# Optimization experiments

Measured on AMD Instinct MI355X. Metric: run time of the kernel, lower is better.

Reference implementation:

```python
import jax, jax.numpy as jnp
import numpy as np

N = 16384        # num nodes
NE = 262144      # num edges (avg degree 16)
IN = 3           # input_dim
H = 128          # hidden_dim
ED = 2           # edge_dim (position differences, 2D coords)
L = 3            # num GNN layers
LAT = 64         # latent_dim
NR = 8192        # num reduced nodes (reduction_factor=0.5)
K = 3            # kNN for interpolation


def _ln(x, g, b, eps=1e-5):
    m = jnp.mean(x, axis=-1, keepdims=True)
    v = jnp.mean((x - m) ** 2, axis=-1, keepdims=True)
    return (x - m) / jnp.sqrt(v + eps) * g + b


def _mlp(x, w1, b1, w2, b2):
    return jax.nn.relu(x @ w1 + b1) @ w2 + b2


def setup_inputs() -> dict:
    key = jax.random.key(0)
    ks = jax.random.split(key, 32)
    def nrm(k, shape, s=0.05):
        return jax.random.normal(k, shape, dtype=jnp.float32) * s
    inp = {}
    inp["x"] = jax.random.normal(ks[0], (N, IN), dtype=jnp.float32)
    inp["node_positions"] = jax.random.uniform(ks[1], (N, 2), dtype=jnp.float32)
    inp["edge_index"] = jax.random.randint(ks[2], (2, NE), 0, N, dtype=jnp.int32)
    # mlp0 + lnm0
    inp["m0_w1"] = nrm(ks[3], (IN, H)); inp["m0_b1"] = jnp.zeros((H,), jnp.float32)
    inp["m0_w2"] = nrm(ks[4], (H, H)); inp["m0_b2"] = jnp.zeros((H,), jnp.float32)
    inp["ln0_g"] = jnp.ones((H,), jnp.float32); inp["ln0_b"] = jnp.zeros((H,), jnp.float32)
    # mlp1 + lnm1 (edge feature transform, edge_dim=2)
    inp["m1_w1"] = nrm(ks[5], (ED, H)); inp["m1_b1"] = jnp.zeros((H,), jnp.float32)
    inp["m1_w2"] = nrm(ks[6], (H, ED)); inp["m1_b2"] = jnp.zeros((ED,), jnp.float32)
    inp["ln1_g"] = jnp.ones((ED,), jnp.float32); inp["ln1_b"] = jnp.zeros((ED,), jnp.float32)
    # GNN layers (stacked over L)
    inp["g_msg_w1"] = nrm(ks[7], (L, 2 * H + ED, H)); inp["g_msg_b1"] = jnp.zeros((L, H), jnp.float32)
    inp["g_msg_w2"] = nrm(ks[8], (L, H, H)); inp["g_msg_b2"] = jnp.zeros((L, H), jnp.float32)
    inp["g_node_w1"] = nrm(ks[9], (L, 2 * H, H)); inp["g_node_b1"] = jnp.zeros((L, H), jnp.float32)
    inp["g_node_w2"] = nrm(ks[10], (L, H, H)); inp["g_node_b2"] = jnp.zeros((L, H), jnp.float32)
    inp["g_edge_w1"] = nrm(ks[11], (L, 2 * H + ED, H)); inp["g_edge_b1"] = jnp.zeros((L, H), jnp.float32)
    inp["g_edge_w2"] = nrm(ks[12], (L, H, ED)); inp["g_edge_b2"] = jnp.zeros((L, ED), jnp.float32)
    inp["g_lnn_g"] = jnp.ones((L, H), jnp.float32); inp["g_lnn_b"] = jnp.zeros((L, H), jnp.float32)
    inp["g_lne_g"] = jnp.ones((L, ED), jnp.float32); inp["g_lne_b"] = jnp.zeros((L, ED), jnp.float32)
    # mlp2 + lnm2
    inp["m2_w1"] = nrm(ks[13], (H, H)); inp["m2_b1"] = jnp.zeros((H,), jnp.float32)
    inp["m2_w2"] = nrm(ks[14], (H, H)); inp["m2_b2"] = jnp.zeros((H,), jnp.float32)
    inp["ln2_g"] = jnp.ones((H,), jnp.float32); inp["ln2_b"] = jnp.zeros((H,), jnp.float32)
    # output_proj
    inp["op_w1"] = nrm(ks[15], (H, H)); inp["op_b1"] = jnp.zeros((H,), jnp.float32)
    inp["op_w2"] = nrm(ks[16], (H, LAT)); inp["op_b2"] = jnp.zeros((LAT,), jnp.float32)
    return inp


def reference(x, edge_index, node_positions,
              m0_w1, m0_b1, m0_w2, m0_b2, ln0_g, ln0_b,
              m1_w1, m1_b1, m1_w2, m1_b2, ln1_g, ln1_b,
              g_msg_w1, g_msg_b1, g_msg_w2, g_msg_b2,
              g_node_w1, g_node_b1, g_node_w2, g_node_b2,
              g_edge_w1, g_edge_b1, g_edge_w2, g_edge_b2,
              g_lnn_g, g_lnn_b, g_lne_g, g_lne_b,
              m2_w1, m2_b1, m2_w2, m2_b2, ln2_g, ln2_b,
              op_w1, op_b1, op_w2, op_b2):
    row, col = edge_index[0], edge_index[1]
    # Stage 1: node encoder  U0 -> U1
    u = _ln(_mlp(x, m0_w1, m0_b1, m0_w2, m0_b2), ln0_g, ln0_b)
    # Stage 2: edge features from positions, E0 -> E1
    e = node_positions[col] - node_positions[row]          # [NE, 2]
    e = _ln(_mlp(e, m1_w1, m1_b1, m1_w2, m1_b2), ln1_g, ln1_b)
    # Stage 3: message-passing layers
    ones = jnp.ones((NE, 1), dtype=u.dtype)
    cnt = jnp.maximum(jax.ops.segment_sum(ones, col, num_segments=N), 1.0)
    for l in range(L):
        msg_in = jnp.concatenate([u[row], u[col], e], axis=-1)   # [NE, 2H+ED]
        m = _mlp(msg_in, g_msg_w1[l], g_msg_b1[l], g_msg_w2[l], g_msg_b2[l])
        agg = jax.ops.segment_sum(m, col, num_segments=N) / cnt  # mean aggregation
        u = _ln(u + _mlp(jnp.concatenate([u, agg], axis=-1),
                         g_node_w1[l], g_node_b1[l], g_node_w2[l], g_node_b2[l]),
                g_lnn_g[l], g_lnn_b[l])
        e = _ln(e + _mlp(jnp.concatenate([u[row], u[col], e], axis=-1),
                         g_edge_w1[l], g_edge_b1[l], g_edge_w2[l], g_edge_b2[l]),
                g_lne_g[l], g_lne_b[l])
    # Stage 4: U2 -> U3
    u3 = _ln(_mlp(u, m2_w1, m2_b1, m2_w2, m2_b2), ln2_g, ln2_b)
    # Stage 5: interpolate onto reduced coordinates (kNN inverse-distance weights)
    idx_r = jnp.floor(jnp.linspace(0.0, N - 1, NR)).astype(jnp.int32)
    x2 = node_positions[idx_r]                               # [NR, 2]
    d2 = (jnp.sum(x2 * x2, axis=1)[:, None]
          + jnp.sum(node_positions * node_positions, axis=1)[None, :]
          - 2.0 * x2 @ node_positions.T)                     # [NR, N]
    d2 = jnp.maximum(d2, 0.0)
    neg_d2, knn = jax.lax.top_k(-d2, K)                      # [NR, K]
    w = 1.0 / (jnp.sqrt(-neg_d2) + 1e-8)
    w = w / jnp.sum(w, axis=1, keepdims=True)
    z_feat = jnp.einsum('nk,nkh->nh', w, u3[knn])            # [NR, H]
    # Stage 6: global mean pool (no batch vector) + output projection
    z = jnp.mean(z_feat, axis=0, keepdims=True)              # [1, H]
    return _mlp(z, op_w1, op_b1, op_w2, op_b2)               # [1, LAT]
```

## Files before the change

kernel.cpp:

```cpp
#include <hip/hip_runtime.h>
#include <cfloat>

#define NN     16384
#define NEDGE  262144
#define HD     128
#define NLAYER 3
#define NRED   8192
#define LATD   64
#define GDIM   32

typedef __attribute__((ext_vector_type(8))) short short8;
typedef __attribute__((ext_vector_type(4))) float f32x4;

__device__ __forceinline__ unsigned short f2bf(float f) {
    union { float f; unsigned u; } v; v.f = f;
    unsigned u = v.u;
    unsigned r = u + 0x7fff + ((u >> 16) & 1);
    return (unsigned short)(r >> 16);
}
__device__ __forceinline__ void unp8(uint4 v, float* f) {
    unsigned w0=v.x, w1=v.y, w2=v.z, w3=v.w;
    f[0]=__uint_as_float(w0<<16); f[1]=__uint_as_float(w0&0xffff0000u);
    f[2]=__uint_as_float(w1<<16); f[3]=__uint_as_float(w1&0xffff0000u);
    f[4]=__uint_as_float(w2<<16); f[5]=__uint_as_float(w2&0xffff0000u);
    f[6]=__uint_as_float(w3<<16); f[7]=__uint_as_float(w3&0xffff0000u);
}
__device__ __forceinline__ unsigned long long umin64(unsigned long long a, unsigned long long b) {
    return a < b ? a : b;
}
__device__ __forceinline__ unsigned long long umax64(unsigned long long a, unsigned long long b) {
    return a < b ? b : a;
}

__device__ __forceinline__ unsigned short pack_std(const float* W, int ksteps, int q) {
    int j    = q & 7;
    int lane = (q >> 3) & 63;
    int ks   = (q >> 9) % ksteps;
    int nt   = q / (ksteps * 512);
    int k = ks*32 + (lane >> 4)*8 + j;
    int n = nt*16 + (lane & 15);
    return f2bf(W[k*128 + n]);
}
__device__ __forceinline__ unsigned short pack_w2e(const float* W, int q) {
    int j    = q & 7;
    int lane = (q >> 3) & 63;
    int ks   = q >> 9;
    int k = ks*32 + (lane >> 4)*8 + j;
    int n = lane & 15;
    return (n < 2) ? f2bf(W[k*2 + n]) : (unsigned short)0;
}

#define PK_TOTAL 448512
__global__ __launch_bounds__(256) void k_pack_all(
    const float* __restrict__ msgw1, const float* __restrict__ msgw2,
    const float* __restrict__ edgew1, const float* __restrict__ nodew1,
    const float* __restrict__ nodew2, const float* __restrict__ edgew2,
    const float* __restrict__ m0w2, const float* __restrict__ m2w1,
    const float* __restrict__ m2w2, unsigned short* __restrict__ P)
{
    int p = blockIdx.x*256 + threadIdx.x;
    if (p >= PK_TOTAL) return;
    unsigned short v;
    if (p < 98304) {
        int l = p / 32768, q = p % 32768;
        v = pack_std(msgw1 + (size_t)l*258*128, 8, q);
    } else if (p < 147456) {
        int t = p - 98304; int l = t / 16384, q = t % 16384;
        v = pack_std(msgw2 + (size_t)l*16384, 4, q);
    } else if (p < 245760) {
        int t = p - 147456; int l = t / 32768, q = t % 32768;
        v = pack_std(edgew1 + (size_t)l*258*128, 8, q);
    } else if (p < 344064) {
        int t = p - 245760; int l = t / 32768, q = t % 32768;
        v = pack_std(nodew1 + (size_t)l*256*128, 8, q);
    } else if (p < 393216) {
        int t = p - 344064; int l = t / 16384, q = t % 16384;
        v = pack_std(nodew2 + (size_t)l*16384, 4, q);
    } else if (p < 399360) {
        int t = p - 393216; int l = t / 2048, q = t % 2048;
        v = pack_w2e(edgew2 + (size_t)l*256, q);
    } else if (p < 415744) {
        v = pack_std(m0w2, 4, p - 399360);
    } else if (p < 432128) {
        v = pack_std(m2w1, 4, p - 415744);
    } else {
        v = pack_std(m2w2, 4, p - 432128);
    }
    P[p] = v;
}

union HUu { unsigned short Hs[64][136]; uint4 UF4[1024]; };

__global__ __launch_bounds__(256) void k_nenc_mfma(
    const float* __restrict__ x,
    const float* __restrict__ w1, const float* __restrict__ b1,
    const unsigned short* __restrict__ W2p, const float* __restrict__ B2,
    const float* __restrict__ lg, const float* __restrict__ lb,
    const unsigned short* __restrict__ mW1p, const float* __restrict__ mB1,
    float* __restrict__ u, unsigned short* __restrict__ u16,
    unsigned short* __restrict__ RM, unsigned short* __restrict__ CM,
    float* __restrict__ agg)
{
    __shared__ float xs[64][4];
    __shared__ float w1s[3][128];
    __shared__ float b1s[128];
    __shared__ HUu HU;
    __shared__ float Rs[64][132];
    __shared__ float red[64][4];
    __shared__ float mstat[64], sstat[64];
    int tid = threadIdx.x;
    int n0  = blockIdx.x * 64;
    {
        float4 z; z.x=0.f; z.y=0.f; z.z=0.f; z.w=0.f;
        for (int t = tid; t < 2048; t += 256)
            *(float4*)(agg + (size_t)(n0 + (t>>5))*HD + (t&31)*4) = z;
    }
    for (int t = tid; t < 384; t += 256) w1s[t >> 7][t & 127] = w1[t];
    if (tid < 128) b1s[tid] = b1[tid];
    for (int t = tid; t < 192; t += 256) xs[t/3][t%3] = x[(size_t)n0*3 + t];
    __syncthreads();
    {
        int m = tid >> 2, p0 = (tid & 3) * 32;
        float x0 = xs[m][0], x1 = xs[m][1], x2 = xs[m][2];
        for (int j = p0; j < p0 + 32; j += 2) {
            float h0 = fmaxf(b1s[j]   + x0*w1s[0][j]   + x1*w1s[1][j]   + x2*w1s[2][j],   0.f);
            float h1 = fmaxf(b1s[j+1] + x0*w1s[0][j+1] + x1*w1s[1][j+1] + x2*w1s[2][j+1], 0.f);
            *(unsigned*)&HU.Hs[m][j] = f2bf(h0) | ((unsigned)f2bf(h1) << 16);
        }
    }
    __syncthreads();

    int lane = tid & 63, wave = tid >> 6;
    int lr = lane & 15, lq = lane >> 4;
    f32x4 acc[8];
    #pragma unroll
    for (int i = 0; i < 8; ++i) acc[i] = (f32x4){0.f,0.f,0.f,0.f};
    for (int ks = 0; ks < 4; ++ks) {
        short8 a0 = *(const short8*)&HU.Hs[ 0 + lr][ks*32 + lq*8];
        short8 a1 = *(const short8*)&HU.Hs[16 + lr][ks*32 + lq*8];
        short8 a2 = *(const short8*)&HU.Hs[32 + lr][ks*32 + lq*8];
        short8 a3 = *(const short8*)&HU.Hs[48 + lr][ks*32 + lq*8];
        short8 b0 = *(const short8*)(W2p + (size_t)(((wave*2+0)*4 + ks)*64 + lane)*8);
        short8 b1v= *(const short8*)(W2p + (size_t)(((wave*2+1)*4 + ks)*64 + lane)*8);
        acc[0] = __builtin_amdgcn_mfma_f32_16x16x32_bf16(a0, b0, acc[0], 0,0,0);
        acc[1] = __builtin_amdgcn_mfma_f32_16x16x32_bf16(a0, b1v, acc[1], 0,0,0);
        acc[2] = __builtin_amdgcn_mfma_f32_16x16x32_bf16(a1, b0, acc[2], 0,0,0);
        acc[3] = __builtin_amdgcn_mfma_f32_16x16x32_bf16(a1, b1v, acc[3], 0,0,0);
        acc[4] = __builtin_amdgcn_mfma_f32_16x16x32_bf16(a2, b0, acc[4], 0,0,0);
        acc[5] = __builtin_amdgcn_mfma_f32_16x16x32_bf16(a2, b1v, acc[5], 0,0,0);
        acc[6] = __builtin_amdgcn_mfma_f32_16x16x32_bf16(a3, b0, acc[6], 0,0,0);
        acc[7] = __builtin_amdgcn_mfma_f32_16x16x32_bf16(a3, b1v, acc[7], 0,0,0);
    }
    #pragma unroll
// ... 5 lines not shown
            f32x4 v = acc[mt*2 + b];
            #pragma unroll
            for (int r = 0; r < 4; ++r) {
                int m = mt*16 + lq*4 + r;
                Rs[m][n] = v[r] + bb;
            }
        }
    }
    __syncthreads();
    {
        int m = tid >> 2, p = tid & 3;
        float s = 0.f;
        #pragma unroll 8
        for (int i = 0; i < 32; ++i) s += Rs[m][p*32 + i];
        red[m][p] = s;
    }
    __syncthreads();
    if (tid < 64) mstat[tid] = (red[tid][0]+red[tid][1]+red[tid][2]+red[tid][3]) * (1.f/HD);
    __syncthreads();
    {
        int m = tid >> 2, p = tid & 3;
        float mm = mstat[m];
        float s = 0.f;
        #pragma unroll 8
        for (int i = 0; i < 32; ++i) { float d = Rs[m][p*32 + i] - mm; s += d*d; }
        red[m][p] = s;
    }
    __syncthreads();
    if (tid < 64) sstat[tid] = sqrtf((red[tid][0]+red[tid][1]+red[tid][2]+red[tid][3]) * (1.f/HD) + 1e-5f);
    __syncthreads();
    for (int t = tid; t < 2048; t += 256) {
        int m = t >> 5, q = t & 31;
        int n = q*4;
        float mm = mstat[m], sd = sstat[m];
        float4 g4 = *(const float4*)(lg + n);
        float4 b4 = *(const float4*)(lb + n);
        float o0 = (Rs[m][n+0]-mm)/sd*g4.x + b4.x;
        float o1 = (Rs[m][n+1]-mm)/sd*g4.y + b4.y;
        float o2 = (Rs[m][n+2]-mm)/sd*g4.z + b4.z;
        float o3 = (Rs[m][n+3]-mm)/sd*g4.w + b4.w;
        float4 fo; fo.x=o0; fo.y=o1; fo.z=o2; fo.w=o3;
        *(float4*)(u + (size_t)(n0+m)*HD + n) = fo;
        uint2 pk; pk.x = f2bf(o0) | (f2bf(o1)<<16); pk.y = f2bf(o2) | (f2bf(o3)<<16);
        *(uint2*)(u16 + (size_t)(n0+m)*HD + n) = pk;
        int ksf = n >> 5, sub = (n >> 3) & 3;
        int slot = (ksf*4 + (m >> 4))*64 + ((m & 15) | (sub << 4));
        unsigned short* UF = (unsigned short*)HU.UF4;
        *(uint2*)&UF[slot*8 + (n & 7)] = pk;
    }
    __syncthreads();

    for (int g = 0; g < 2; ++g) {
        int ksOff = g*4;
        unsigned short* Out = g ? CM : RM;
        #pragma unroll
        for (int i = 0; i < 8; ++i) acc[i] = (f32x4){0.f,0.f,0.f,0.f};
        for (int ks = 0; ks < 4; ++ks) {
            short8 a0 = *(const short8*)&HU.UF4[(ks*4+0)*64 + lane];
            short8 a1 = *(const short8*)&HU.UF4[(ks*4+1)*64 + lane];
            short8 a2 = *(const short8*)&HU.UF4[(ks*4+2)*64 + lane];
            short8 a3 = *(const short8*)&HU.UF4[(ks*4+3)*64 + lane];
            short8 b0 = *(const short8*)(mW1p + (size_t)(((wave*2+0)*8 + ksOff + ks)*64 + lane)*8);
            short8 b1v= *(const short8*)(mW1p + (size_t)(((wave*2+1)*8 + ksOff + ks)*64 + lane)*8);
            acc[0] = __builtin_amdgcn_mfma_f32_16x16x32_bf16(a0, b0, acc[0], 0,0,0);
            acc[1] = __builtin_amdgcn_mfma_f32_16x16x32_bf16(a0, b1v, acc[1], 0,0,0);
            acc[2] = __builtin_amdgcn_mfma_f32_16x16x32_bf16(a1, b0, acc[2], 0,0,0);
            acc[3] = __builtin_amdgcn_mfma_f32_16x16x32_bf16(a1, b1v, acc[3], 0,0,0);
            acc[4] = __builtin_amdgcn_mfma_f32_16x16x32_bf16(a2, b0, acc[4], 0,0,0);
            acc[5] = __builtin_amdgcn_mfma_f32_16x16x32_bf16(a2, b1v, acc[5], 0,0,0);
            acc[6] = __builtin_amdgcn_mfma_f32_16x16x32_bf16(a3, b0, acc[6], 0,0,0);
            acc[7] = __builtin_amdgcn_mfma_f32_16x16x32_bf16(a3, b1v, acc[7], 0,0,0);
        }
        #pragma unroll
        for (int b = 0; b < 2; ++b) {
            int n = (wave*2 + b)*16 + lr;
            float bb = g ? mB1[n] : 0.f;
            #pragma unroll
            for (int mt = 0; mt < 4; ++mt) {
                f32x4 v = acc[mt*2 + b];
                #pragma unroll
                for (int r = 0; r < 4; ++r) {
                    int rowp = n0 + mt*16 + lq*4 + r;
                    unsigned hv = f2bf(v[r] + bb);
                    unsigned ph = (unsigned)__shfl_xor((int)hv, 1, 64);
                    if (!(lr & 1))
                        *(unsigned*)&Out[(size_t)rowp*HD + n] = hv | (ph << 16);
                }
            }
        }
    }
}

__global__ __launch_bounds__(256) void k_edge_enc(
    const float* __restrict__ pos, const int* __restrict__ row, const int* __restrict__ col,
    const float* __restrict__ w1, const float* __restrict__ b1,
    const float* __restrict__ w2, const float* __restrict__ b2,
    const float* __restrict__ lg, const float* __restrict__ lb,
    float* __restrict__ ef)
{
    int e = blockIdx.x*256 + threadIdx.x;
    if (e >= NEDGE) return;
    int r = row[e], c = col[e];
    float e0 = pos[c*2]   - pos[r*2];
    float e1 = pos[c*2+1] - pos[r*2+1];
    float o0 = b2[0], o1 = b2[1];
    for (int j = 0; j < HD; ++j) {
        float h = fmaxf(e0*w1[j] + e1*w1[HD+j] + b1[j], 0.f);
        o0 += h*w2[j*2];
        o1 += h*w2[j*2+1];
    }
    float m  = 0.5f*(o0 + o1);
    float d0 = o0 - m, d1 = o1 - m;
    float v  = 0.5f*(d0*d0 + d1*d1);
    float sd = sqrtf(v + 1e-5f);
    ef[e*2]   = d0/sd*lg[0] + lb[0];
    ef[e*2+1] = d1/sd*lg[1] + lb[1];
}

__global__ void k_count2(const int* __restrict__ col, const float* __restrict__ pos,
                         int* __restrict__ cnt, int* __restrict__ gcnt)
{
    int e = blockIdx.x*256 + threadIdx.x;
    if (e < NEDGE) atomicAdd(&cnt[col[e]], 1);
    if (e < NN) {
        int cx = min(max((int)(pos[e*2]  *(float)GDIM), 0), GDIM-1);
        int cy = min(max((int)(pos[e*2+1]*(float)GDIM), 0), GDIM-1);
        atomicAdd(&gcnt[cy*GDIM + cx], 1);
    }
}

__global__ __launch_bounds__(256) void k_scan2(
    const int* __restrict__ cnt, int* __restrict__ head,
    const int* __restrict__ gcnt, int* __restrict__ gstart, int* __restrict__ ghead)
{
    __shared__ int ls[257];
    int tid = threadIdx.x;
    if (blockIdx.x == 0) {
        int base = tid * (NN/256);
        int s = 0;
// ... 52 lines not shown
    const float2* __restrict__ psort, const int* __restrict__ pidx,
    float* __restrict__ coef)
{
    int r = blockIdx.x*256 + threadIdx.x;
    int ni = (int)(2.0*r + (double)r/8191.0);
    float qx = pos[ni*2], qy = pos[ni*2+1];
    float s2 = qx*qx + qy*qy;
    int cx = min(max((int)(qx*(float)GDIM), 0), GDIM-1);
    int cy = min(max((int)(qy*(float)GDIM), 0), GDIM-1);
    const float h = 1.f/(float)GDIM;
    unsigned long long k0 = ~0ull, k1 = ~0ull, k2 = ~0ull;
    for (int rr = 0; rr < GDIM; ++rr) {
        if (rr > 0 && k2 != ~0ull) {
            float bound = rr*h;
            float d3 = __uint_as_float((unsigned)(k2 >> 32));
            if (d3 < bound*bound*0.9999f) break;
        }
        int ylo = max(cy-rr, 0), yhi = min(cy+rr, GDIM-1);
        int xlo = max(cx-rr, 0), xhi = min(cx+rr, GDIM-1);
        for (int gy = ylo; gy <= yhi; ++gy) {
            bool yedge = (gy == cy-rr) || (gy == cy+rr);
            for (int gx = xlo; gx <= xhi; ++gx) {
                if (!yedge && gx != cx-rr && gx != cx+rr) continue;
                int cell = gy*GDIM + gx;
                int s = gstart[cell], e = gstart[cell+1];
                for (; s < e; ++s) {
                    float2 p = psort[s];
                    float sc = p.x*p.x + p.y*p.y;
                    float dt = qx*p.x + qy*p.y;
                    float d2 = fmaxf(s2 + sc - 2.f*dt, 0.f);
                    unsigned long long key =
                        ((unsigned long long)__float_as_uint(d2) << 32) | (unsigned)pidx[s];
                    unsigned long long a0 = umin64(k0, key);
                    unsigned long long a1 = umin64(k1, umax64(k0, key));
                    unsigned long long a2 = umin64(k2, umax64(k1, key));
                    k0 = a0; k1 = a1; k2 = a2;
                }
            }
        }
    }
    float d0 = __uint_as_float((unsigned)(k0 >> 32));
    float d1 = __uint_as_float((unsigned)(k1 >> 32));
    float d2 = __uint_as_float((unsigned)(k2 >> 32));
    float w0 = 1.f/(sqrtf(d0) + 1e-8f);
    float w1 = 1.f/(sqrtf(d1) + 1e-8f);
    float w2 = 1.f/(sqrtf(d2) + 1e-8f);
    float ws = w0 + w1 + w2;
    atomicAdd(&coef[(int)(unsigned)(k0 & 0xffffffffu)], w0/ws);
    atomicAdd(&coef[(int)(unsigned)(k1 & 0xffffffffu)], w1/ws);
    atomicAdd(&coef[(int)(unsigned)(k2 & 0xffffffffu)], w2/ws);
}

__global__ __launch_bounds__(256) void k_hagg0(
    const unsigned short* __restrict__ RM, const unsigned short* __restrict__ CM,
    const float* __restrict__ ef,
    const int* __restrict__ row, const int* __restrict__ col,
    const int* __restrict__ perm,
    const float* __restrict__ mW1e,
    float* __restrict__ agg)
{
    __shared__ float Ms[64][132];
    __shared__ float Pw[256];
    __shared__ float Es[64][2];
    __shared__ int colS[64], rowS[64], eS[64];
    int tid = threadIdx.x;
    int e0  = blockIdx.x * 64;
    if (tid < 64) {
        int e = perm[e0 + tid];
        eS[tid] = e; colS[tid] = col[e]; rowS[tid] = row[e];
    }
    for (int t = tid; t < 256; t += 256) Pw[t] = mW1e[t];
    __syncthreads();
    if (tid < 128) { Es[tid>>1][tid&1] = ef[(size_t)eS[tid>>1]*2 + (tid&1)]; }
    __syncthreads();

    int mP = (tid >> 6)*16 + (tid & 15);
    int ccB = ((tid & 63) >> 4)*8;
    float e0v = Es[mP][0], e1v = Es[mP][1];
    #pragma unroll
    for (int s4 = 0; s4 < 4; ++s4) {
        int cc = s4*32 + ccB;
        uint4 ra = *(const uint4*)(RM + (size_t)rowS[mP]*HD + cc);
        uint4 cb = *(const uint4*)(CM + (size_t)colS[mP]*HD + cc);
        float rf[8], cf[8];
        unp8(ra, rf); unp8(cb, cf);
        float4 o0, o1;
        o0.x = fmaxf(rf[0]+cf[0]+e0v*Pw[cc+0]+e1v*Pw[128+cc+0], 0.f);
        o0.y = fmaxf(rf[1]+cf[1]+e0v*Pw[cc+1]+e1v*Pw[128+cc+1], 0.f);
        o0.z = fmaxf(rf[2]+cf[2]+e0v*Pw[cc+2]+e1v*Pw[128+cc+2], 0.f);
        o0.w = fmaxf(rf[3]+cf[3]+e0v*Pw[cc+3]+e1v*Pw[128+cc+3], 0.f);
        o1.x = fmaxf(rf[4]+cf[4]+e0v*Pw[cc+4]+e1v*Pw[128+cc+4], 0.f);
        o1.y = fmaxf(rf[5]+cf[5]+e0v*Pw[cc+5]+e1v*Pw[128+cc+5], 0.f);
        o1.z = fmaxf(rf[6]+cf[6]+e0v*Pw[cc+6]+e1v*Pw[128+cc+6], 0.f);
        o1.w = fmaxf(rf[7]+cf[7]+e0v*Pw[cc+7]+e1v*Pw[128+cc+7], 0.f);
        *(float4*)&Ms[mP][cc]   = o0;
        *(float4*)&Ms[mP][cc+4] = o1;
    }
    __syncthreads();

    {
        int n = tid & 127, hh = tid >> 7;
        int m0 = hh*32;
        float accv = 0.f;
        int cur = colS[m0];
        for (int m = m0; m < m0 + 32; ++m) {
            int cm = colS[m];
            if (cm != cur) {
                atomicAdd(&agg[(size_t)cur*HD + n], accv);
                accv = 0.f; cur = cm;
            }
            accv += Ms[m][n];
        }
        atomicAdd(&agg[(size_t)cur*HD + n], accv);
    }
}

union MsHFu { uint4 HF4[1024]; float Ms[64][132]; };

__global__ __launch_bounds__(256) void k_edgemsg2(
    const unsigned short* __restrict__ RE, const unsigned short* __restrict__ CE,
    const unsigned short* __restrict__ RM, const unsigned short* __restrict__ CM,
    float* __restrict__ ef,
    const int* __restrict__ row, const int* __restrict__ col,
    const int* __restrict__ perm,
    const float* __restrict__ eW1e,
    const unsigned short* __restrict__ eW2p, const float* __restrict__ eB2,
    const float* __restrict__ elg, const float* __restrict__ elb,
    const float* __restrict__ mW1e,
    float* __restrict__ agg, int writeEf)
{
    __shared__ MsHFu MU;
    __shared__ float Pew[256], Pmw[256];
    __shared__ float Es[64][2];
    __shared__ int colS[64], rowS[64], eS[64];
    int tid = threadIdx.x;
    int e0  = blockIdx.x * 64;
    if (tid < 64) {
        int e = perm[e0 + tid];
        eS[tid] = e; colS[tid] = col[e]; rowS[tid] = row[e];
    }
    for (int t = tid; t < 256; t += 256) { Pew[t] = eW1e[t]; Pmw[t] = mW1e[t]; }
    __syncthreads();

    int mP = (tid >> 6)*16 + (tid & 15);
    int ccB = ((tid & 63) >> 4)*8;
    uint4 regR[4], regC[4];
    #pragma unroll
    for (int s4 = 0; s4 < 4; ++s4) {
        int cc = s4*32 + ccB;
        regR[s4] = *(const uint4*)(RM + (size_t)rowS[mP]*HD + cc);
        regC[s4] = *(const uint4*)(CM + (size_t)colS[mP]*HD + cc);
    }
    if (tid < 128) { Es[tid>>1][tid&1] = ef[(size_t)eS[tid>>1]*2 + (tid&1)]; }
    __syncthreads();

    int lane = tid & 63, wave = tid >> 6;
    int lr = lane & 15, lq = lane >> 4;

    {
        float e0v = Es[mP][0], e1v = Es[mP][1];
        #pragma unroll
        for (int s4 = 0; s4 < 4; ++s4) {
            int s = tid + s4*256;
            int cc = s4*32 + ccB;
            uint4 ra = *(const uint4*)(RE + (size_t)rowS[mP]*HD + cc);
            uint4 cb = *(const uint4*)(CE + (size_t)colS[mP]*HD + cc);
            float rf[8], cf[8];
            unp8(ra, rf); unp8(cb, cf);
            unsigned short hb[8];
            #pragma unroll
            for (int j = 0; j < 8; ++j) {
                int n = cc + j;
                float o = rf[j] + cf[j] + e0v*Pew[n] + e1v*Pew[128+n];
                hb[j] = f2bf(fmaxf(o, 0.f));
            }
            uint4 pk;
            pk.x = hb[0] | ((unsigned)hb[1]<<16); pk.y = hb[2] | ((unsigned)hb[3]<<16);
            pk.z = hb[4] | ((unsigned)hb[5]<<16); pk.w = hb[6] | ((unsigned)hb[7]<<16);
            MU.HF4[s] = pk;
        }
    }
    __syncthreads();

    f32x4 a2 = (f32x4){0.f,0.f,0.f,0.f};
    for (int ks = 0; ks < 4; ++ks) {
        short8 a = *(const short8*)&MU.HF4[(ks*4 + wave)*64 + lane];
        short8 b = *(const short8*)(eW2p + (size_t)(ks*64 + lane)*8);
        a2 = __builtin_amdgcn_mfma_f32_16x16x32_bf16(a, b, a2, 0,0,0);
    }
    if (lr < 2) {
        int d = lr;
        float bb = eB2[d];
        float gg = elg[d], bl = elb[d];
        #pragma unroll
        for (int r = 0; r < 4; ++r) {
            int m = wave*16 + lq*4 + r;
            float rv = Es[m][d] + a2[r] + bb;
            float other = __shfl_xor(rv, 1, 64);
            float mm = 0.5f*(rv + other);
            float dr = rv - mm, dro = other - mm;
            float vv = 0.5f*(dr*dr + dro*dro);
            float outv = dr / sqrtf(vv + 1e-5f) * gg + bl;
            Es[m][d] = outv;
            if (writeEf) ef[(size_t)eS[m]*2 + d] = outv;
        }
    }
    __syncthreads();

    {
        float e0v = Es[mP][0], e1v = Es[mP][1];
        #pragma unroll
        for (int s4 = 0; s4 < 4; ++s4) {
            int cc = s4*32 + ccB;
            float rf[8], cf[8];
            unp8(regR[s4], rf); unp8(regC[s4], cf);
            float4 o0, o1;
            o0.x = fmaxf(rf[0]+cf[0]+e0v*Pmw[cc+0]+e1v*Pmw[128+cc+0], 0.f);
            o0.y = fmaxf(rf[1]+cf[1]+e0v*Pmw[cc+1]+e1v*Pmw[128+cc+1], 0.f);
            o0.z = fmaxf(rf[2]+cf[2]+e0v*Pmw[cc+2]+e1v*Pmw[128+cc+2], 0.f);
            o0.w = fmaxf(rf[3]+cf[3]+e0v*Pmw[cc+3]+e1v*Pmw[128+cc+3], 0.f);
            o1.x = fmaxf(rf[4]+cf[4]+e0v*Pmw[cc+4]+e1v*Pmw[128+cc+4], 0.f);
            o1.y = fmaxf(rf[5]+cf[5]+e0v*Pmw[cc+5]+e1v*Pmw[128+cc+5], 0.f);
            o1.z = fmaxf(rf[6]+cf[6]+e0v*Pmw[cc+6]+e1v*Pmw[128+cc+6], 0.f);
            o1.w = fmaxf(rf[7]+cf[7]+e0v*Pmw[cc+7]+e1v*Pmw[128+cc+7], 0.f);
            *(float4*)&MU.Ms[mP][cc]   = o0;
            *(float4*)&MU.Ms[mP][cc+4] = o1;
        }
    }
    __syncthreads();

    {
        int n = tid & 127, hh = tid >> 7;
        int m0 = hh*32;
        float accv = 0.f;
        int cur = colS[m0];
        for (int m = m0; m < m0 + 32; ++m) {
            int cm = colS[m];
            if (cm != cur) {
                atomicAdd(&agg[(size_t)cur*HD + n], accv);
                accv = 0.f; cur = cm;
            }
            accv += MU.Ms[m][n];
        }
        atomicAdd(&agg[(size_t)cur*HD + n], accv);
    }
}

union XRu { unsigned short Xs[64][264]; float Rs[64][132]; };

__global__ __launch_bounds__(256) void k_node_mfma(
    float* __restrict__ u, unsigned short* __restrict__ u16,
    float* __restrict__ agg, const int* __restrict__ cnt,
    const unsigned short* __restrict__ W1p, const float* __restrict__ B1,
    const unsigned short* __restrict__ W2p, const float* __restrict__ B2,
    const float* __restrict__ lg, const float* __restrict__ lb,
    const unsigned short* __restrict__ mW2pC, const float* __restrict__ mB2C,
    int doExtra,
    const unsigned short* __restrict__ eW1p, const float* __restrict__ eB1c,
    const unsigned short* __restrict__ mW1pN, const float* __restrict__ mB1N,
    unsigned short* __restrict__ RE, unsigned short* __restrict__ CE,
    unsigned short* __restrict__ RM, unsigned short* __restrict__ CM)
{
    __shared__ XRu XR;
    __shared__ HUu HU;
    __shared__ float red[64][4];
    __shared__ float mstat[64], sstat[64];
    __shared__ float invS[64], fS[64];
    int tid = threadIdx.x;
    int n0  = blockIdx.x * 64;
    for (int t = tid; t < 1024; t += 256) {
        int el = t >> 4, kc = t & 15;
        uint4 v = *(const uint4*)(u16 + (size_t)(n0+el)*HD + kc*8);
        *(uint4*)&XR.Xs[el][kc*8] = v;
    }
    if (tid < 64) {
        int c = cnt[n0 + tid];
        invS[tid] = 1.f / fmaxf((float)c, 1.f);
        fS[tid] = (c > 0) ? 1.f : 0.f;
    }
    for (int t = tid; t < 1024; t += 256) {
        int lane_s = t & 63, ksmt = t >> 6;
        int ks = ksmt >> 2, mt = ksmt & 3;
        int el = mt*16 + (lane_s & 15);
        int cc = ks*32 + (lane_s >> 4)*8;
        const float* src = agg + (size_t)(n0+el)*HD + cc;
        float4 a = *(const float4*)src;
        float4 b = *(const float4*)(src + 4);
        uint4 pk;
        pk.x = f2bf(a.x) | ((unsigned)f2bf(a.y) << 16);
        pk.y = f2bf(a.z) | ((unsigned)f2bf(a.w) << 16);
        pk.z = f2bf(b.x) | ((unsigned)f2bf(b.y) << 16);
        pk.w = f2bf(b.z) | ((unsigned)f2bf(b.w) << 16);
        HU.UF4[t] = pk;
    }
    __syncthreads();

    int lane = tid & 63, wave = tid >> 6;
    int lr = lane & 15, lq = lane >> 4;
    f32x4 acc[8];

    #pragma unroll
    for (int i = 0; i < 8; ++i) acc[i] = (f32x4){0.f,0.f,0.f,0.f};
    for (int ks = 0; ks < 4; ++ks) {
        short8 a0 = *(const short8*)&HU.UF4[(ks*4+0)*64 + lane];
        short8 a1 = *(const short8*)&HU.UF4[(ks*4+1)*64 + lane];
        short8 a2 = *(const short8*)&HU.UF4[(ks*4+2)*64 + lane];
        short8 a3 = *(const short8*)&HU.UF4[(ks*4+3)*64 + lane];
        short8 b0 = *(const short8*)(mW2pC + (size_t)(((wave*2+0)*4 + ks)*64 + lane)*8);
        short8 b1 = *(const short8*)(mW2pC + (size_t)(((wave*2+1)*4 + ks)*64 + lane)*8);
        acc[0] = __builtin_amdgcn_mfma_f32_16x16x32_bf16(a0, b0, acc[0], 0,0,0);
        acc[1] = __builtin_amdgcn_mfma_f32_16x16x32_bf16(a0, b1, acc[1], 0,0,0);
        acc[2] = __builtin_amdgcn_mfma_f32_16x16x32_bf16(a1, b0, acc[2], 0,0,0);
        acc[3] = __builtin_amdgcn_mfma_f32_16x16x32_bf16(a1, b1, acc[3], 0,0,0);
        acc[4] = __builtin_amdgcn_mfma_f32_16x16x32_bf16(a2, b0, acc[4], 0,0,0);
// ... 91 lines not shown
    {
        int m = tid >> 2, p = tid & 3;
        float s = 0.f;
        #pragma unroll 8
        for (int i = 0; i < 32; ++i) s += XR.Rs[m][p*32 + i];
        red[m][p] = s;
    }
    __syncthreads();
    if (tid < 64) mstat[tid] = (red[tid][0]+red[tid][1]+red[tid][2]+red[tid][3]) * (1.f/HD);
    __syncthreads();
    {
        int m = tid >> 2, p = tid & 3;
        float mm = mstat[m];
        float s = 0.f;
        #pragma unroll 8
        for (int i = 0; i < 32; ++i) { float d = XR.Rs[m][p*32 + i] - mm; s += d*d; }
        red[m][p] = s;
    }
    __syncthreads();
    if (tid < 64) sstat[tid] = sqrtf((red[tid][0]+red[tid][1]+red[tid][2]+red[tid][3]) * (1.f/HD) + 1e-5f);
    __syncthreads();
    for (int t = tid; t < 2048; t += 256) {
        int m = t >> 5, q = t & 31;
        int n = q*4;
        float mm = mstat[m], sd = sstat[m];
        float4 g4 = *(const float4*)(lg + n);
        float4 b4 = *(const float4*)(lb + n);
        float o0 = (XR.Rs[m][n+0]-mm)/sd*g4.x + b4.x;
        float o1 = (XR.Rs[m][n+1]-mm)/sd*g4.y + b4.y;
        float o2 = (XR.Rs[m][n+2]-mm)/sd*g4.z + b4.z;
        float o3 = (XR.Rs[m][n+3]-mm)/sd*g4.w + b4.w;
        float4 fo; fo.x=o0; fo.y=o1; fo.z=o2; fo.w=o3;
        *(float4*)(u + (size_t)(n0+m)*HD + n) = fo;
        uint2 pk; pk.x = f2bf(o0) | (f2bf(o1)<<16); pk.y = f2bf(o2) | (f2bf(o3)<<16);
        *(uint2*)(u16 + (size_t)(n0+m)*HD + n) = pk;
        if (doExtra) {
            int ksf = n >> 5, sub = (n >> 3) & 3;
            int slot = (ksf*4 + (m >> 4))*64 + ((m & 15) | (sub << 4));
            unsigned short* UF = (unsigned short*)HU.UF4;
            *(uint2*)&UF[slot*8 + (n & 7)] = pk;
        }
    }
    {
        float4 z; z.x=0.f; z.y=0.f; z.z=0.f; z.w=0.f;
        for (int t = tid; t < 2048; t += 256)
            *(float4*)(agg + (size_t)(n0 + (t>>5))*HD + (t&31)*4) = z;
    }
    if (!doExtra) return;
    __syncthreads();

    for (int g = 0; g < 4; ++g) {
        const unsigned short* Bp = (g < 2) ? eW1p : mW1pN;
        int ksOff = (g & 1) * 4;
        unsigned short* Out = (g == 0) ? RE : (g == 1) ? CE : (g == 2) ? RM : CM;
        const float* bias = (g == 1) ? eB1c : (g == 3) ? mB1N : (const float*)nullptr;
        #pragma unroll
        for (int i = 0; i < 8; ++i) acc[i] = (f32x4){0.f,0.f,0.f,0.f};
        for (int ks = 0; ks < 4; ++ks) {
            short8 a0 = *(const short8*)&HU.UF4[(ks*4+0)*64 + lane];
            short8 a1 = *(const short8*)&HU.UF4[(ks*4+1)*64 + lane];
            short8 a2 = *(const short8*)&HU.UF4[(ks*4+2)*64 + lane];
            short8 a3 = *(const short8*)&HU.UF4[(ks*4+3)*64 + lane];
            short8 b0 = *(const short8*)(Bp + (size_t)(((wave*2+0)*8 + ksOff + ks)*64 + lane)*8);
            short8 b1 = *(const short8*)(Bp + (size_t)(((wave*2+1)*8 + ksOff + ks)*64 + lane)*8);
            acc[0] = __builtin_amdgcn_mfma_f32_16x16x32_bf16(a0, b0, acc[0], 0,0,0);
            acc[1] = __builtin_amdgcn_mfma_f32_16x16x32_bf16(a0, b1, acc[1], 0,0,0);
            acc[2] = __builtin_amdgcn_mfma_f32_16x16x32_bf16(a1, b0, acc[2], 0,0,0);
            acc[3] = __builtin_amdgcn_mfma_f32_16x16x32_bf16(a1, b1, acc[3], 0,0,0);
            acc[4] = __builtin_amdgcn_mfma_f32_16x16x32_bf16(a2, b0, acc[4], 0,0,0);
            acc[5] = __builtin_amdgcn_mfma_f32_16x16x32_bf16(a2, b1, acc[5], 0,0,0);
            acc[6] = __builtin_amdgcn_mfma_f32_16x16x32_bf16(a3, b0, acc[6], 0,0,0);
            acc[7] = __builtin_amdgcn_mfma_f32_16x16x32_bf16(a3, b1, acc[7], 0,0,0);
        }
        #pragma unroll
        for (int b = 0; b < 2; ++b) {
            int n = (wave*2 + b)*16 + lr;
            float bb = bias ? bias[n] : 0.f;
            #pragma unroll
            for (int mt = 0; mt < 4; ++mt) {
                f32x4 v = acc[mt*2 + b];
                #pragma unroll
                for (int r = 0; r < 4; ++r) {
                    int rowp = n0 + mt*16 + lq*4 + r;
                    unsigned hv = f2bf(v[r] + bb);
                    unsigned ph = (unsigned)__shfl_xor((int)hv, 1, 64);
                    if (!(lr & 1))
                        *(unsigned*)&Out[(size_t)rowp*HD + n] = hv | (ph << 16);
                }
            }
        }
    }
}

__global__ __launch_bounds__(256) void k_m2_mfma(
    const unsigned short* __restrict__ u16,
    const unsigned short* __restrict__ W1p, const float* __restrict__ B1,
    const unsigned short* __restrict__ W2p, const float* __restrict__ B2,
    const float* __restrict__ lg, const float* __restrict__ lb,
    const float* __restrict__ coef, float* __restrict__ partial)
{
    __shared__ unsigned short Xs[64][136];
    __shared__ unsigned short Hs[64][136];
    __shared__ float Rs[64][132];
    __shared__ float red[64][4];
    __shared__ float mstat[64], sstat[64];
    __shared__ float zp[HD];
    int tid = threadIdx.x;
    int n0  = blockIdx.x * 64;
    if (tid < HD) zp[tid] = 0.f;
    for (int t = tid; t < 1024; t += 256) {
        int el = t >> 4, kc = t & 15;
        uint4 v = *(const uint4*)(u16 + (size_t)(n0+el)*HD + kc*8);
        *(uint4*)&Xs[el][kc*8] = v;
    }
    __syncthreads();

    int lane = tid & 63, wave = tid >> 6;
    int lr = lane & 15, lq = lane >> 4;
    f32x4 acc[8];
    #pragma unroll
    for (int i = 0; i < 8; ++i) acc[i] = (f32x4){0.f,0.f,0.f,0.f};
    for (int ks = 0; ks < 4; ++ks) {
        short8 a0 = *(const short8*)&Xs[ 0 + lr][ks*32 + lq*8];
        short8 a1 = *(const short8*)&Xs[16 + lr][ks*32 + lq*8];
        short8 a2 = *(const short8*)&Xs[32 + lr][ks*32 + lq*8];
        short8 a3 = *(const short8*)&Xs[48 + lr][ks*32 + lq*8];
        short8 b0 = *(const short8*)(W1p + (size_t)(((wave*2+0)*4 + ks)*64 + lane)*8);
        short8 b1 = *(const short8*)(W1p + (size_t)(((wave*2+1)*4 + ks)*64 + lane)*8);
        acc[0] = __builtin_amdgcn_mfma_f32_16x16x32_bf16(a0, b0, acc[0], 0,0,0);
        acc[1] = __builtin_amdgcn_mfma_f32_16x16x32_bf16(a0, b1, acc[1], 0,0,0);
        acc[2] = __builtin_amdgcn_mfma_f32_16x16x32_bf16(a1, b0, acc[2], 0,0,0);
        acc[3] = __builtin_amdgcn_mfma_f32_16x16x32_bf16(a1, b1, acc[3], 0,0,0);
        acc[4] = __builtin_amdgcn_mfma_f32_16x16x32_bf16(a2, b0, acc[4], 0,0,0);
        acc[5] = __builtin_amdgcn_mfma_f32_16x16x32_bf16(a2, b1, acc[5], 0,0,0);
        acc[6] = __builtin_amdgcn_mfma_f32_16x16x32_bf16(a3, b0, acc[6], 0,0,0);
        acc[7] = __builtin_amdgcn_mfma_f32_16x16x32_bf16(a3, b1, acc[7], 0,0,0);
    }
    #pragma unroll
    for (int b = 0; b < 2; ++b) {
        int n = (wave*2 + b)*16 + lr;
// ... 137 lines not shown
    const float* ln1_g = (const float*)d_in[13];
    const float* ln1_b = (const float*)d_in[14];
    const float* g_msg_w1  = (const float*)d_in[15];
    const float* g_msg_b1  = (const float*)d_in[16];
    const float* g_msg_w2  = (const float*)d_in[17];
    const float* g_msg_b2  = (const float*)d_in[18];
    const float* g_node_w1 = (const float*)d_in[19];
    const float* g_node_b1 = (const float*)d_in[20];
    const float* g_node_w2 = (const float*)d_in[21];
    const float* g_node_b2 = (const float*)d_in[22];
    const float* g_edge_w1 = (const float*)d_in[23];
    const float* g_edge_b1 = (const float*)d_in[24];
    const float* g_edge_w2 = (const float*)d_in[25];
    const float* g_edge_b2 = (const float*)d_in[26];
    const float* g_lnn_g   = (const float*)d_in[27];
    const float* g_lnn_b   = (const float*)d_in[28];
    const float* g_lne_g   = (const float*)d_in[29];
    const float* g_lne_b   = (const float*)d_in[30];
    const float* m2_w1 = (const float*)d_in[31];
    const float* m2_b1 = (const float*)d_in[32];
    const float* m2_w2 = (const float*)d_in[33];
    const float* m2_b2 = (const float*)d_in[34];
    const float* ln2_g = (const float*)d_in[35];
    const float* ln2_b = (const float*)d_in[36];
    const float* op_w1 = (const float*)d_in[37];
    const float* op_b1 = (const float*)d_in[38];
    const float* op_w2 = (const float*)d_in[39];
    const float* op_b2 = (const float*)d_in[40];

    float* u    = (float*)d_ws;
    float* ef   = u + (size_t)NN*HD;
    float* agg  = ef + (size_t)NEDGE*2;
    int*   cnt  = (int*)(agg + (size_t)NN*HD);
    int*   gcnt = cnt + NN;
    float* coef = (float*)(gcnt + 1024);
    int*   head = (int*)(coef + NN);
    int*   perm = head + NN;
    float* partial = (float*)(perm + NEDGE);
    int*   gstart = (int*)(partial + (NN/64)*HD);
    int*   ghead  = gstart + 1026;
    int*   pidx   = ghead + 1024;
    float2* psort = (float2*)(pidx + NN);
    unsigned short* u16 = (unsigned short*)(psort + NN);
    unsigned short* packs = u16 + (size_t)NN*HD;
    unsigned short* msgW1p  = packs;
    unsigned short* msgW2p  = packs + 98304;
    unsigned short* edgeW1p = packs + 147456;
    unsigned short* nodeW1p = packs + 245760;
    unsigned short* nodeW2p = packs + 344064;
    unsigned short* edgeW2p = packs + 393216;
    unsigned short* m0w2p   = packs + 399360;
    unsigned short* m2w1p   = packs + 415744;
    unsigned short* m2w2p   = packs + 432128;
    unsigned short* RE = packs + PK_TOTAL;
    unsigned short* CE = RE + (size_t)NN*HD;
    unsigned short* RM = CE + (size_t)NN*HD;
    unsigned short* CM = RM + (size_t)NN*HD;

    k_pack_all<<<(PK_TOTAL + 255)/256, 256, 0, stream>>>(
        g_msg_w1, g_msg_w2, g_edge_w1, g_node_w1, g_node_w2, g_edge_w2,
        m0_w2, m2_w1, m2_w2, packs);

    hipMemsetAsync(cnt, 0, (NN + 1024 + NN)*sizeof(int), stream);

    k_nenc_mfma<<<NN/64, 256, 0, stream>>>(x, m0_w1, m0_b1, m0w2p, m0_b2, ln0_g, ln0_b,
                                           msgW1p, g_msg_b1, u, u16, RM, CM, agg);
    k_edge_enc<<<NEDGE/256, 256, 0, stream>>>(pos, row, col, m1_w1, m1_b1, m1_w2, m1_b2,
                                              ln1_g, ln1_b, ef);

    k_count2<<<NEDGE/256, 256, 0, stream>>>(col, pos, cnt, gcnt);
    k_scan2<<<2, 256, 0, stream>>>(cnt, head, gcnt, gstart, ghead);
    k_scatter2<<<NEDGE/256, 256, 0, stream>>>(col, pos, head, perm, ghead, psort, pidx);
    k_knnsel<<<NRED/256, 256, 0, stream>>>(pos, gstart, psort, pidx, coef);

    k_hagg0<<<NEDGE/64, 256, 0, stream>>>(RM, CM, ef, row, col, perm,
        g_msg_w1 + 256*HD, agg);
    k_node_mfma<<<NN/64, 256, 0, stream>>>(u, u16, agg, cnt,
        nodeW1p, g_node_b1, nodeW2p, g_node_b2, g_lnn_g, g_lnn_b,
        msgW2p, g_msg_b2,
        1, edgeW1p + 0*32768, g_edge_b1 + 0*HD, msgW1p + 1*32768, g_msg_b1 + 1*HD,
        RE, CE, RM, CM);

    for (int l = 0; l < NLAYER-1; ++l) {
        k_edgemsg2<<<NEDGE/64, 256, 0, stream>>>(RE, CE, RM, CM, ef, row, col, perm,
            g_edge_w1 + (size_t)l*258*HD + 256*HD,
            edgeW2p + l*2048, g_edge_b2 + l*2, g_lne_g + l*2, g_lne_b + l*2,
            g_msg_w1 + (size_t)(l+1)*258*HD + 256*HD,
            agg, (l == 0) ? 1 : 0);
        int doExtra = (l == 0) ? 1 : 0;
        k_node_mfma<<<NN/64, 256, 0, stream>>>(u, u16, agg, cnt,
            nodeW1p + (l+1)*32768, g_node_b1 + (l+1)*HD,
            nodeW2p + (l+1)*16384, g_node_b2 + (l+1)*HD,
            g_lnn_g + (l+1)*HD, g_lnn_b + (l+1)*HD,
            msgW2p + (l+1)*16384, g_msg_b2 + (l+1)*HD,
            doExtra, edgeW1p + 1*32768, g_edge_b1 + 1*HD, msgW1p + 2*32768, g_msg_b1 + 2*HD,
            RE, CE, RM, CM);
    }

    k_m2_mfma<<<NN/64, 256, 0, stream>>>(u16, m2w1p, m2_b1, m2w2p, m2_b2, ln2_g, ln2_b,
                                         coef, partial);
    k_out<<<1, 128, 0, stream>>>(partial, op_w1, op_b1, op_w2, op_b2, (float*)d_out);
}
```

Baseline: 450.0 us.

## Interleave edge and message projections per node and swizzle edge-block order

Merges the separate RE/RM and CE/CM bf16 projection buffers into two interleaved tables (row and col) with a 256-element stride, so each node's edge and message projections share one contiguous 512-byte row. Gathers in the edge kernels then touch adjacent memory for both halves, which should improve cache-line and TLB locality. Edge-block indices are also remapped with an XCD-style swizzle ((bid&7)*512 + bid>>3), which changes which blocks run together on each chip partition and so how the L2 caches are shared. The swizzle assumes exactly 4096 blocks.

After: 463.1 us. 2.9% more time.

```diff
diff --git a/kernel.cpp b/kernel.cpp
--- a/kernel.cpp
+++ b/kernel.cpp
@@ -8,6 +8,7 @@
 #define NRED   8192
 #define LATD   64
 #define GDIM   32
+#define RCS    256
 
 typedef __attribute__((ext_vector_type(8))) short short8;
 typedef __attribute__((ext_vector_type(4))) float f32x4;
@@ -98,7 +99,7 @@
     const float* __restrict__ lg, const float* __restrict__ lb,
     const unsigned short* __restrict__ mW1p, const float* __restrict__ mB1,
     float* __restrict__ u, unsigned short* __restrict__ u16,
-    unsigned short* __restrict__ RM, unsigned short* __restrict__ CM,
+    unsigned short* __restrict__ RT, unsigned short* __restrict__ CT,
     float* __restrict__ agg)
 {
     __shared__ float xs[64][4];
@@ -210,7 +211,7 @@
 
     for (int g = 0; g < 2; ++g) {
         int ksOff = g*4;
-        unsigned short* Out = g ? CM : RM;
+        unsigned short* Out = (g ? CT : RT) + 128;
         #pragma unroll
         for (int i = 0; i < 8; ++i) acc[i] = (f32x4){0.f,0.f,0.f,0.f};
         for (int ks = 0; ks < 4; ++ks) {
@@ -242,7 +243,7 @@
                     unsigned hv = f2bf(v[r] + bb);
                     unsigned ph = (unsigned)__shfl_xor((int)hv, 1, 64);
                     if (!(lr & 1))
-                        *(unsigned*)&Out[(size_t)rowp*HD + n] = hv | (ph << 16);
+                        *(unsigned*)&Out[(size_t)rowp*RCS + n] = hv | (ph << 16);
                 }
             }
         }
@@ -401,7 +402,7 @@
 }
 
 __global__ __launch_bounds__(256) void k_hagg0(
-    const unsigned short* __restrict__ RM, const unsigned short* __restrict__ CM,
+    const unsigned short* __restrict__ RT, const unsigned short* __restrict__ CT,
     const float* __restrict__ ef,
     const int* __restrict__ row, const int* __restrict__ col,
     const int* __restrict__ perm,
@@ -413,7 +414,8 @@
     __shared__ float Es[64][2];
     __shared__ int colS[64], rowS[64], eS[64];
     int tid = threadIdx.x;
-    int e0  = blockIdx.x * 64;
+    int bid = blockIdx.x;
+    int e0  = ((bid & 7)*512 + (bid >> 3)) * 64;
     if (tid < 64) {
         int e = perm[e0 + tid];
         eS[tid] = e; colS[tid] = col[e]; rowS[tid] = row[e];
@@ -426,11 +428,13 @@
     int mP = (tid >> 6)*16 + (tid & 15);
     int ccB = ((tid & 63) >> 4)*8;
     float e0v = Es[mP][0], e1v = Es[mP][1];
+    const unsigned short* rbase = RT + (size_t)rowS[mP]*RCS + 128;
+    const unsigned short* cbase = CT + (size_t)colS[mP]*RCS + 128;
     #pragma unroll
     for (int s4 = 0; s4 < 4; ++s4) {
         int cc = s4*32 + ccB;
-        uint4 ra = *(const uint4*)(RM + (size_t)rowS[mP]*HD + cc);
-        uint4 cb = *(const uint4*)(CM + (size_t)colS[mP]*HD + cc);
+        uint4 ra = *(const uint4*)(rbase + cc);
+        uint4 cb = *(const uint4*)(cbase + cc);
         float rf[8], cf[8];
         unp8(ra, rf); unp8(cb, cf);
         float4 o0, o1;
@@ -467,8 +471,7 @@
 union MsHFu { uint4 HF4[1024]; float Ms[64][132]; };
 
 __global__ __launch_bounds__(256) void k_edgemsg2(
-    const unsigned short* __restrict__ RE, const unsigned short* __restrict__ CE,
-    const unsigned short* __restrict__ RM, const unsigned short* __restrict__ CM,
+    const unsigned short* __restrict__ RT, const unsigned short* __restrict__ CT,
     float* __restrict__ ef,
     const int* __restrict__ row, const int* __restrict__ col,
     const int* __restrict__ perm,
@@ -483,7 +486,8 @@
     __shared__ float Es[64][2];
     __shared__ int colS[64], rowS[64], eS[64];
     int tid = threadIdx.x;
-    int e0  = blockIdx.x * 64;
+    int bid = blockIdx.x;
+    int e0  = ((bid & 7)*512 + (bid >> 3)) * 64;
     if (tid < 64) {
         int e = perm[e0 + tid];
         eS[tid] = e; colS[tid] = col[e]; rowS[tid] = row[e];
@@ -493,12 +497,14 @@
 
     int mP = (tid >> 6)*16 + (tid & 15);
     int ccB = ((tid & 63) >> 4)*8;
+    const unsigned short* rbase = RT + (size_t)rowS[mP]*RCS;
+    const unsigned short* cbase = CT + (size_t)colS[mP]*RCS;
     uint4 regR[4], regC[4];
     #pragma unroll
     for (int s4 = 0; s4 < 4; ++s4) {
         int cc = s4*32 + ccB;
-        regR[s4] = *(const uint4*)(RM + (size_t)rowS[mP]*HD + cc);
-        regC[s4] = *(const uint4*)(CM + (size_t)colS[mP]*HD + cc);
+        regR[s4] = *(const uint4*)(rbase + 128 + cc);
+        regC[s4] = *(const uint4*)(cbase + 128 + cc);
     }
     if (tid < 128) { Es[tid>>1][tid&1] = ef[(size_t)eS[tid>>1]*2 + (tid&1)]; }
     __syncthreads();
@@ -512,8 +518,8 @@
         for (int s4 = 0; s4 < 4; ++s4) {
             int s = tid + s4*256;
             int cc = s4*32 + ccB;
-            uint4 ra = *(const uint4*)(RE + (size_t)rowS[mP]*HD + cc);
-            uint4 cb = *(const uint4*)(CE + (size_t)colS[mP]*HD + cc);
+            uint4 ra = *(const uint4*)(rbase + cc);
+            uint4 cb = *(const uint4*)(cbase + cc);
             float rf[8], cf[8];
             unp8(ra, rf); unp8(cb, cf);
             unsigned short hb[8];
@@ -607,8 +613,7 @@
     int doExtra,
     const unsigned short* __restrict__ eW1p, const float* __restrict__ eB1c,
     const unsigned short* __restrict__ mW1pN, const float* __restrict__ mB1N,
-    unsigned short* __restrict__ RE, unsigned short* __restrict__ CE,
-    unsigned short* __restrict__ RM, unsigned short* __restrict__ CM)
+    unsigned short* __restrict__ RT, unsigned short* __restrict__ CT)
 {
     __shared__ XRu XR;
     __shared__ HUu HU;
@@ -806,7 +811,7 @@
     for (int g = 0; g < 4; ++g) {
         const unsigned short* Bp = (g < 2) ? eW1p : mW1pN;
         int ksOff = (g & 1) * 4;
-        unsigned short* Out = (g == 0) ? RE : (g == 1) ? CE : (g == 2) ? RM : CM;
+        unsigned short* Out = ((g & 1) ? CT : RT) + ((g < 2) ? 0 : 128);
         const float* bias = (g == 1) ? eB1c : (g == 3) ? mB1N : (const float*)nullptr;
         #pragma unroll
         for (int i = 0; i < 8; ++i) acc[i] = (f32x4){0.f,0.f,0.f,0.f};
@@ -839,7 +844,7 @@
                     unsigned hv = f2bf(v[r] + bb);
                     unsigned ph = (unsigned)__shfl_xor((int)hv, 1, 64);
                     if (!(lr & 1))
-                        *(unsigned*)&Out[(size_t)rowp*HD + n] = hv | (ph << 16);
+                        *(unsigned*)&Out[(size_t)rowp*RCS + n] = hv | (ph << 16);
                 }
             }
         }
@@ -1083,10 +1088,8 @@
     unsigned short* m0w2p   = packs + 399360;
     unsigned short* m2w1p   = packs + 415744;
     unsigned short* m2w2p   = packs + 432128;
-    unsigned short* RE = packs + PK_TOTAL;
-    unsigned short* CE = RE + (size_t)NN*HD;
-    unsigned short* RM = CE + (size_t)NN*HD;
-    unsigned short* CM = RM + (size_t)NN*HD;
+    unsigned short* RT = packs + PK_TOTAL;
+    unsigned short* CT = RT + (size_t)NN*RCS;
 
     k_pack_all<<<(PK_TOTAL + 255)/256, 256, 0, stream>>>(
         g_msg_w1, g_msg_w2, g_edge_w1, g_node_w1, g_node_w2, g_edge_w2,
@@ -1095,7 +1098,7 @@
     hipMemsetAsync(cnt, 0, (NN + 1024 + NN)*sizeof(int), stream);
 
     k_nenc_mfma<<<NN/64, 256, 0, stream>>>(x, m0_w1, m0_b1, m0w2p, m0_b2, ln0_g, ln0_b,
-                                           msgW1p, g_msg_b1, u, u16, RM, CM, agg);
+                                           msgW1p, g_msg_b1, u, u16, RT, CT, agg);
     k_edge_enc<<<NEDGE/256, 256, 0, stream>>>(pos, row, col, m1_w1, m1_b1, m1_w2, m1_b2,
                                               ln1_g, ln1_b, ef);
 
@@ -1104,16 +1107,16 @@
     k_scatter2<<<NEDGE/256, 256, 0, stream>>>(col, pos, head, perm, ghead, psort, pidx);
     k_knnsel<<<NRED/256, 256, 0, stream>>>(pos, gstart, psort, pidx, coef);
 
-    k_hagg0<<<NEDGE/64, 256, 0, stream>>>(RM, CM, ef, row, col, perm,
+    k_hagg0<<<NEDGE/64, 256, 0, stream>>>(RT, CT, ef, row, col, perm,
         g_msg_w1 + 256*HD, agg);
     k_node_mfma<<<NN/64, 256, 0, stream>>>(u, u16, agg, cnt,
         nodeW1p, g_node_b1, nodeW2p, g_node_b2, g_lnn_g, g_lnn_b,
         msgW2p, g_msg_b2,
         1, edgeW1p + 0*32768, g_edge_b1 + 0*HD, msgW1p + 1*32768, g_msg_b1 + 1*HD,
-        RE, CE, RM, CM);
+        RT, CT);
 
     for (int l = 0; l < NLAYER-1; ++l) {
-        k_edgemsg2<<<NEDGE/64, 256, 0, stream>>>(RE, CE, RM, CM, ef, row, col, perm,
+        k_edgemsg2<<<NEDGE/64, 256, 0, stream>>>(RT, CT, ef, row, col, perm,
             g_edge_w1 + (size_t)l*258*HD + 256*HD,
             edgeW2p + l*2048, g_edge_b2 + l*2, g_lne_g + l*2, g_lne_b + l*2,
             g_msg_w1 + (size_t)(l+1)*258*HD + 256*HD,
@@ -1125,7 +1128,7 @@
             g_lnn_g + (l+1)*HD, g_lnn_b + (l+1)*HD,
             msgW2p + (l+1)*16384, g_msg_b2 + (l+1)*HD,
             doExtra, edgeW1p + 1*32768, g_edge_b1 + 1*HD, msgW1p + 2*32768, g_msg_b1 + 2*HD,
-            RE, CE, RM, CM);
+            RT, CT);
     }
 
     k_m2_mfma<<<NN/64, 256, 0, stream>>>(u16, m2w1p, m2_b1, m2w2p, m2_b2, ln2_g, ln2_b,
```
